# Performance work log

Measured on AMD Instinct MI355X. Metric: run time of the kernel, lower is better.

Reference implementation:

```python
import jax, jax.numpy as jnp
import numpy as np

N_X = 50000      # real nodes
N_MOTIF = 10000  # motif nodes
N = N_X + N_MOTIF
E = 1_920_000    # edges (avg degree 32)
NFEAT = 512
NHID = 256
PAD_N = 65536


def setup_inputs() -> dict:
    key = jax.random.key(0)
    ks = jax.random.split(key, 12)
    x = jax.random.normal(ks[0], (N_X, NFEAT), dtype=jnp.float32)
    motif_emb = jax.random.normal(ks[1], (N_MOTIF, NFEAT), dtype=jnp.float32)
    adj_rows = jax.random.randint(ks[2], (E,), 0, N)
    adj_cols = jax.random.randint(ks[3], (E,), 0, N)
    adj_vals = jax.random.uniform(ks[4], (E,), dtype=jnp.float32)
    # unique scatter positions (torch output[pos_idx]=x with distinct indices)
    pos_idx = jax.random.permutation(ks[5], PAD_N)[:N_X]
    # GraphConvolution params (pygcn style: support = x@W; out = spmm(adj, support) + b)
    s1 = 1.0 / np.sqrt(NHID)
    w1 = jax.random.uniform(ks[6], (NFEAT, NHID), minval=-s1, maxval=s1, dtype=jnp.float32)
    b1 = jax.random.uniform(ks[7], (NHID,), minval=-s1, maxval=s1, dtype=jnp.float32)
    w2 = jax.random.uniform(ks[8], (NHID, NHID), minval=-s1, maxval=s1, dtype=jnp.float32)
    b2 = jax.random.uniform(ks[9], (NHID,), minval=-s1, maxval=s1, dtype=jnp.float32)
    w3 = jax.random.uniform(ks[10], (NHID, NHID), minval=-s1, maxval=s1, dtype=jnp.float32)
    b3 = jax.random.uniform(ks[11], (NHID,), minval=-s1, maxval=s1, dtype=jnp.float32)
    return {"x": x, "motif_emb": motif_emb, "adj_rows": adj_rows, "adj_cols": adj_cols,
            "adj_vals": adj_vals, "pos_idx": pos_idx, "pad_n": PAD_N,
            "w1": w1, "b1": b1, "w2": w2, "b2": b2, "w3": w3, "b3": b3}


def _gcn_layer(h, rows, cols, vals, w, b):
    support = h @ w                                   # [N, nhid]
    msgs = vals[:, None] * support[cols]              # [E, nhid]
    agg = jax.ops.segment_sum(msgs, rows, num_segments=N)  # spmm(adj, support)
    return jax.nn.relu(agg + b)


def reference(x, motif_emb, adj_rows, adj_cols, adj_vals, pos_idx, pad_n,
              w1, b1, w2, b2, w3, b3):
    h = jnp.concatenate((x, motif_emb), axis=0)       # [N, nfeat]
    h = _gcn_layer(h, adj_rows, adj_cols, adj_vals, w1, b1)
    # dropout is identity in eval mode
    h = _gcn_layer(h, adj_rows, adj_cols, adj_vals, w2, b2)
    h = _gcn_layer(h, adj_rows, adj_cols, adj_vals, w3, b3)
    h = h[:N_X]                                       # drop motif nodes
    output = jnp.zeros((pad_n, h.shape[1]), dtype=h.dtype)
    output = output.at[pos_idx].set(h)                # irregular scatter-assign
    return output
```

## Files before the change

### kernel.cpp

```cpp
#include <hip/hip_runtime.h>

#define N_TOTAL 60000
#define N_X     50000
#define N_EDGE  1920000
#define NFEAT   512
#define NHID    256
#define SLOTS   96

typedef __attribute__((ext_vector_type(8))) short bf16x8;
typedef __attribute__((ext_vector_type(4))) float f32x4;
typedef __attribute__((ext_vector_type(4))) unsigned u32x4;

__device__ __forceinline__ unsigned short f2bf(float f) {
    unsigned u = __float_as_uint(f);
    unsigned r = (u + 0x7FFFu + ((u >> 16) & 1u)) >> 16;
    return (unsigned short)r;
}
__device__ __forceinline__ float bf_lo(unsigned u) { return __uint_as_float(u << 16); }
__device__ __forceinline__ float bf_hi(unsigned u) { return __uint_as_float(u & 0xFFFF0000u); }

__global__ __launch_bounds__(256)
void cvt_w_all_kernel(const float* __restrict__ w1, const float* __restrict__ w2,
                      const float* __restrict__ w3, short* __restrict__ w1T,
                      short* __restrict__ w2T, short* __restrict__ w3T)
{
    int n = blockIdx.x;
    for (int k = threadIdx.x; k < NFEAT; k += 256)
        w1T[(size_t)n * NFEAT + k] = (short)f2bf(w1[(size_t)k * NHID + n]);
    for (int k = threadIdx.x; k < NHID; k += 256)
        w2T[(size_t)n * NHID + k] = (short)f2bf(w2[(size_t)k * NHID + n]);
    for (int k = threadIdx.x; k < NHID; k += 256)
        w3T[(size_t)n * NHID + k] = (short)f2bf(w3[(size_t)k * NHID + n]);
}

#define LDA 40

template<bool AF32>
__global__ __launch_bounds__(256)
void gemm_bt_kernel(const float* __restrict__ Af, const float* __restrict__ A2f, int split,
                    const short* __restrict__ Ab, const short* __restrict__ BT,
                    short* __restrict__ C, int M, int K)
{
    __shared__ short As[128 * LDA];
    __shared__ short Bs[128 * LDA];
    const int t    = threadIdx.x;
    const int lane = t & 63;
    const int wave = t >> 6;
    const int wm   = wave & 1;
    const int wn   = wave >> 1;
    const int l16  = lane & 15;
    const int quad = lane >> 4;
    const int bm   = blockIdx.x * 128;
    const int bn   = blockIdx.y * 128;

    f32x4 acc[4][4] = {};

    const int srow = t >> 2;
    const int sch  = t & 3;
    const int frow = t >> 1;
    const int fh   = t & 1;

    for (int kk = 0; kk < K; kk += 32) {
        if (AF32) {
            int row = bm + frow;
            float4 v0 = {}, v1 = {}, v2 = {}, v3 = {};
            if (row < M) {
                const float* src = (row < split) ? (Af + (size_t)row * K)
                                                 : (A2f + (size_t)(row - split) * K);
                const float4* p = (const float4*)(src + kk + fh * 16);
                v0 = p[0]; v1 = p[1]; v2 = p[2]; v3 = p[3];
            }
            short* dst = &As[frow * LDA + fh * 16];
            short tmp[16] = {
                (short)f2bf(v0.x), (short)f2bf(v0.y), (short)f2bf(v0.z), (short)f2bf(v0.w),
                (short)f2bf(v1.x), (short)f2bf(v1.y), (short)f2bf(v1.z), (short)f2bf(v1.w),
                (short)f2bf(v2.x), (short)f2bf(v2.y), (short)f2bf(v2.z), (short)f2bf(v2.w),
                (short)f2bf(v3.x), (short)f2bf(v3.y), (short)f2bf(v3.z), (short)f2bf(v3.w)};
            *(bf16x8*)(dst)     = *(const bf16x8*)&tmp[0];
            *(bf16x8*)(dst + 8) = *(const bf16x8*)&tmp[8];
        } else {
            bf16x8 va0 = {}, va1 = {};
            int r0 = bm + srow, r1 = bm + srow + 64;
            if (r0 < M) va0 = *(const bf16x8*)(Ab + (size_t)r0 * K + kk + sch * 8);
            if (r1 < M) va1 = *(const bf16x8*)(Ab + (size_t)r1 * K + kk + sch * 8);
            *(bf16x8*)&As[srow * LDA + sch * 8]        = va0;
            *(bf16x8*)&As[(srow + 64) * LDA + sch * 8] = va1;
        }
        {
            bf16x8 vb0 = *(const bf16x8*)(BT + (size_t)(bn + srow) * K + kk + sch * 8);
            bf16x8 vb1 = *(const bf16x8*)(BT + (size_t)(bn + srow + 64) * K + kk + sch * 8);
            *(bf16x8*)&Bs[srow * LDA + sch * 8]        = vb0;
            *(bf16x8*)&Bs[(srow + 64) * LDA + sch * 8] = vb1;
        }
        __syncthreads();

        bf16x8 af[4], bfr[4];
        #pragma unroll
        for (int i = 0; i < 4; i++) {
            af[i]  = *(const bf16x8*)&As[(wm * 64 + i * 16 + l16) * LDA + quad * 8];
            bfr[i] = *(const bf16x8*)&Bs[(wn * 64 + i * 16 + l16) * LDA + quad * 8];
        }
        #pragma unroll
        for (int i = 0; i < 4; i++)
            #pragma unroll
            for (int j = 0; j < 4; j++)
                acc[i][j] = __builtin_amdgcn_mfma_f32_16x16x32_bf16(af[i], bfr[j], acc[i][j], 0, 0, 0);
        __syncthreads();
    }

    #pragma unroll
    for (int i = 0; i < 4; i++) {
        #pragma unroll
        for (int r = 0; r < 4; r++) {
            int row = bm + wm * 64 + i * 16 + quad * 4 + r;
            if (row < M) {
                #pragma unroll
                for (int j = 0; j < 4; j++) {
                    int col = bn + wn * 64 + j * 16 + l16;
                    __builtin_nontemporal_store((short)f2bf(acc[i][j][r]),
                                                C + (size_t)row * NHID + col);
                }
            }
        }
    }
}

__global__ __launch_bounds__(256)
void init_cursor_kernel(int* __restrict__ cursor)
{
    int i = blockIdx.x * 256 + threadIdx.x;
    if (i < N_TOTAL) cursor[i] = i * SLOTS;
}

__global__ __launch_bounds__(256)
void scatter_edges_kernel(const int* __restrict__ rows, const int* __restrict__ cols,
                          const float* __restrict__ vals, int* __restrict__ cursor,
                          unsigned* __restrict__ edges)
{
    const int b = blockIdx.x;
    const int g = b & 7;
    const int i = (b >> 3) * 256 + threadIdx.x;
    const int lo = g * (N_TOTAL / 8);
    const int hi = lo + (N_TOTAL / 8);
    int r = __builtin_nontemporal_load(&rows[i]);
    if (r >= lo && r < hi) {
        unsigned rec = (unsigned)cols[i] | ((unsigned)f2bf(vals[i]) << 16);
        int p = atomicAdd(&cursor[r], 1);
        edges[p] = rec;
    }
}

template<int MODE>
__global__ __launch_bounds__(64)
void spmm_relu_kernel(const int* __restrict__ row_end, const unsigned* __restrict__ edges,
                      const u32x4* __restrict__ support, const float* __restrict__ bias,
                      u32x4* __restrict__ out_bf, float* __restrict__ out_f32,
                      const int* __restrict__ pos)
{
    __shared__ unsigned s_edge[64];
    const int r  = blockIdx.x;
    const int t  = threadIdx.x;
    const int eh = t >> 5;
    const int fl = t & 31;
    const int start = r * SLOTS;
    const int end   = row_end[r];
    const u32x4* __restrict__ sb = support + fl;

    float a[8] = {}, b2[8] = {};
    for (int base = start; base < end; base += 64) {
        int j = base + t;
        if (j < end) s_edge[t] = __builtin_nontemporal_load(&edges[j]);
        __syncthreads();
        int cnt = min(64, end - base);
        int i = eh;
        for (; i + 2 < cnt; i += 4) {
            unsigned e0 = s_edge[i], e1 = s_edge[i + 2];
            u32x4 u0 = sb[(size_t)(e0 & 0xFFFFu) * 32];
            u32x4 u1 = sb[(size_t)(e1 & 0xFFFFu) * 32];
            float v0 = bf_hi(e0), v1 = bf_hi(e1);
            #pragma unroll
            for (int k = 0; k < 4; k++) {
                a[2*k]      += v0 * bf_lo(u0[k]);
                a[2*k + 1]  += v0 * bf_hi(u0[k]);
                b2[2*k]     += v1 * bf_lo(u1[k]);
                b2[2*k + 1] += v1 * bf_hi(u1[k]);
            }
        }
        for (; i < cnt; i += 2) {
            unsigned e0 = s_edge[i];
            u32x4 u0 = sb[(size_t)(e0 & 0xFFFFu) * 32];
            float v0 = bf_hi(e0);
            #pragma unroll
            for (int k = 0; k < 4; k++) {
                a[2*k]     += v0 * bf_lo(u0[k]);
                a[2*k + 1] += v0 * bf_hi(u0[k]);
            }
        }
        __syncthreads();
    }

    const f32x4* bb = (const f32x4*)bias + fl * 2;
    f32x4 bv0 = bb[0], bv1 = bb[1];
    float o[8];
    #pragma unroll
    for (int k = 0; k < 8; k++) {
        float s = a[k] + b2[k];
        s += __shfl_xor(s, 32, 64);
        float bk = (k < 4) ? bv0[k] : bv1[k - 4];
        o[k] = fmaxf(s + bk, 0.f);
    }
    if (t < 32) {
        if (MODE == 1) {
            f32x4 q0 = {o[0], o[1], o[2], o[3]};
            f32x4 q1 = {o[4], o[5], o[6], o[7]};
            f32x4* dst = (f32x4*)out_f32 + (size_t)pos[r] * 64 + fl * 2;
            __builtin_nontemporal_store(q0, dst);
            __builtin_nontemporal_store(q1, dst + 1);
        } else {
            u32x4 q;
            #pragma unroll
            for (int k = 0; k < 4; k++)
                q[k] = (unsigned)f2bf(o[2*k]) | ((unsigned)f2bf(o[2*k + 1]) << 16);
            __builtin_nontemporal_store(q, out_bf + (size_t)r * 32 + fl);
        }
    }
}

extern "C" void kernel_launch(void* const* d_in, const int* in_sizes, int n_in,
                              void* d_out, int out_size, void* d_ws, size_t ws_size,
                              hipStream_t stream)
{
    const float* x     = (const float*)d_in[0];
    const float* motif = (const float*)d_in[1];
    const int*   rows  = (const int*)d_in[2];
    const int*   cols  = (const int*)d_in[3];
    const float* vals  = (const float*)d_in[4];
    const int*   pos   = (const int*)d_in[5];
    const float* w1 = (const float*)d_in[7];
    const float* b1 = (const float*)d_in[8];
    const float* w2 = (const float*)d_in[9];
    const float* b2 = (const float*)d_in[10];
    const float* w3 = (const float*)d_in[11];
    const float* b3 = (const float*)d_in[12];
    (void)ws_size; (void)n_in; (void)in_sizes;

    char* ws = (char*)d_ws;
    size_t off = 0;
    short* h_bf     = (short*)(ws + off); off += (size_t)N_TOTAL * NHID * 2;
    short* support  = (short*)(ws + off); off += (size_t)N_TOTAL * NHID * 2;
    short* w1T      = (short*)(ws + off); off += (size_t)NHID * NFEAT * 2;
    short* w2T      = (short*)(ws + off); off += (size_t)NHID * NHID * 2;
    short* w3T      = (short*)(ws + off); off += (size_t)NHID * NHID * 2;
    int* cursor     = (int*)(ws + off);   off += 60032 * 4;
    unsigned* edges = (unsigned*)(ws + off); off += (size_t)N_TOTAL * SLOTS * 4;

    hipMemsetAsync(d_out, 0, (size_t)out_size * sizeof(float), stream);
    cvt_w_all_kernel<<<NHID, 256, 0, stream>>>(w1, w2, w3, w1T, w2T, w3T);
    init_cursor_kernel<<<(N_TOTAL + 255) / 256, 256, 0, stream>>>(cursor);
    scatter_edges_kernel<<<(N_EDGE / 256) * 8, 256, 0, stream>>>(rows, cols, vals, cursor, edges);

    dim3 ggrid((N_TOTAL + 127) / 128, NHID / 128);

    gemm_bt_kernel<true><<<ggrid, 256, 0, stream>>>(x, motif, N_X, nullptr, w1T, support, N_TOTAL, NFEAT);
    spmm_relu_kernel<0><<<N_TOTAL, 64, 0, stream>>>(cursor, edges, (const u32x4*)support, b1,
                                                    (u32x4*)h_bf, nullptr, nullptr);
    gemm_bt_kernel<false><<<ggrid, 256, 0, stream>>>(nullptr, nullptr, 0, h_bf, w2T, support, N_TOTAL, NHID);
    spmm_relu_kernel<0><<<N_TOTAL, 64, 0, stream>>>(cursor, edges, (const u32x4*)support, b2,
                                                    (u32x4*)h_bf, nullptr, nullptr);
    gemm_bt_kernel<false><<<ggrid, 256, 0, stream>>>(nullptr, nullptr, 0, h_bf, w3T, support, N_TOTAL, NHID);
    spmm_relu_kernel<1><<<N_X, 64, 0, stream>>>(cursor, edges, (const u32x4*)support, b3,
                                                nullptr, (float*)d_out, pos);
}
```

Measured before the change: 745.0 us.

## Pack four rows per SpMM block, use wave-local sync, unroll gather by four

The SpMM kernel now runs four rows per 256-thread block, one wavefront per row. Each wave has its own shared edge buffer, and block barriers are replaced with s_waitcnt fences. The gather loop is unrolled to four edges per half-wave so more loads are in flight. The aim is to cut launch and barrier overhead from 60k tiny blocks and to improve memory-level parallelism. The cost is higher register pressure. Correctness now rests on wave-synchronous assumptions: the write to shared memory followed by reads in the same wave, and the hazard where the buffer is reused before all lanes have read it.

Result: no change. 743.9 us (-0.1%).

```diff
diff --git a/kernel.cpp b/kernel.cpp
--- a/kernel.cpp
+++ b/kernel.cpp
@@ -151,33 +151,42 @@
 }
 
 template<int MODE>
-__global__ __launch_bounds__(64)
+__global__ __launch_bounds__(256)
 void spmm_relu_kernel(const int* __restrict__ row_end, const unsigned* __restrict__ edges,
                       const u32x4* __restrict__ support, const float* __restrict__ bias,
                       u32x4* __restrict__ out_bf, float* __restrict__ out_f32,
-                      const int* __restrict__ pos)
-{
-    __shared__ unsigned s_edge[64];
-    const int r  = blockIdx.x;
-    const int t  = threadIdx.x;
-    const int eh = t >> 5;
-    const int fl = t & 31;
+                      const int* __restrict__ pos, int nrows)
+{
+    __shared__ unsigned s_edge[4][64];
+    const int wave = threadIdx.x >> 6;
+    const int lane = threadIdx.x & 63;
+    const int r    = blockIdx.x * 4 + wave;
+    if (r >= nrows) return;
+    const int eh = lane >> 5;
+    const int fl = lane & 31;
     const int start = r * SLOTS;
     const int end   = row_end[r];
     const u32x4* __restrict__ sb = support + fl;
 
     float a[8] = {}, b2[8] = {};
     for (int base = start; base < end; base += 64) {
-        int j = base + t;
-        if (j < end) s_edge[t] = __builtin_nontemporal_load(&edges[j]);
-        __syncthreads();
+        int j = base + lane;
+        asm volatile("s_waitcnt lgkmcnt(0)" ::: "memory");
+        if (j < end) s_edge[wave][lane] = __builtin_nontemporal_load(&edges[j]);
+        asm volatile("s_waitcnt lgkmcnt(0)" ::: "memory");
+        __builtin_amdgcn_sched_barrier(0);
         int cnt = min(64, end - base);
         int i = eh;
-        for (; i + 2 < cnt; i += 4) {
-            unsigned e0 = s_edge[i], e1 = s_edge[i + 2];
+        for (; i + 6 < cnt; i += 8) {
+            unsigned e0 = s_edge[wave][i];
+            unsigned e1 = s_edge[wave][i + 2];
+            unsigned e2 = s_edge[wave][i + 4];
+            unsigned e3 = s_edge[wave][i + 6];
             u32x4 u0 = sb[(size_t)(e0 & 0xFFFFu) * 32];
             u32x4 u1 = sb[(size_t)(e1 & 0xFFFFu) * 32];
-            float v0 = bf_hi(e0), v1 = bf_hi(e1);
+            u32x4 u2 = sb[(size_t)(e2 & 0xFFFFu) * 32];
+            u32x4 u3 = sb[(size_t)(e3 & 0xFFFFu) * 32];
+            float v0 = bf_hi(e0), v1 = bf_hi(e1), v2 = bf_hi(e2), v3 = bf_hi(e3);
             #pragma unroll
             for (int k = 0; k < 4; k++) {
                 a[2*k]      += v0 * bf_lo(u0[k]);
@@ -185,9 +194,29 @@
                 b2[2*k]     += v1 * bf_lo(u1[k]);
                 b2[2*k + 1] += v1 * bf_hi(u1[k]);
             }
+            #pragma unroll
+            for (int k = 0; k < 4; k++) {
+                a[2*k]      += v2 * bf_lo(u2[k]);
+                a[2*k + 1]  += v2 * bf_hi(u2[k]);
+                b2[2*k]     += v3 * bf_lo(u3[k]);
+                b2[2*k + 1] += v3 * bf_hi(u3[k]);
+            }
+        }
+        for (; i + 2 < cnt; i += 4) {
+            unsigned e0 = s_edge[wave][i], e1 = s_edge[wave][i + 2];
+            u32x4 u0 = sb[(size_t)(e0 & 0xFFFFu) * 32];
+            u32x4 u1 = sb[(size_t)(e1 & 0xFFFFu) * 32];
+            float v0 = bf_hi(e0), v1 = bf_hi(e1);
+            #pragma unroll
+            for (int k = 0; k < 4; k++) {
+                a[2*k]      += v0 * bf_lo(u0[k]);
+                a[2*k + 1]  += v0 * bf_hi(u0[k]);
+                b2[2*k]     += v1 * bf_lo(u1[k]);
+                b2[2*k + 1] += v1 * bf_hi(u1[k]);
+            }
         }
         for (; i < cnt; i += 2) {
-            unsigned e0 = s_edge[i];
+            unsigned e0 = s_edge[wave][i];
             u32x4 u0 = sb[(size_t)(e0 & 0xFFFFu) * 32];
             float v0 = bf_hi(e0);
             #pragma unroll
@@ -196,7 +225,6 @@
                 a[2*k + 1] += v0 * bf_hi(u0[k]);
             }
         }
-        __syncthreads();
     }
 
     const f32x4* bb = (const f32x4*)bias + fl * 2;
@@ -209,7 +237,7 @@
         float bk = (k < 4) ? bv0[k] : bv1[k - 4];
         o[k] = fmaxf(s + bk, 0.f);
     }
-    if (t < 32) {
+    if (lane < 32) {
         if (MODE == 1) {
             f32x4 q0 = {o[0], o[1], o[2], o[3]};
             f32x4 q1 = {o[4], o[5], o[6], o[7]};
@@ -262,12 +290,12 @@
     dim3 ggrid((N_TOTAL + 127) / 128, NHID / 128);
 
     gemm_bt_kernel<true><<<ggrid, 256, 0, stream>>>(x, motif, N_X, nullptr, w1T, support, N_TOTAL, NFEAT);
-    spmm_relu_kernel<0><<<N_TOTAL, 64, 0, stream>>>(cursor, edges, (const u32x4*)support, b1,
-                                                    (u32x4*)h_bf, nullptr, nullptr);
+    spmm_relu_kernel<0><<<(N_TOTAL + 3) / 4, 256, 0, stream>>>(cursor, edges, (const u32x4*)support, b1,
+                                                               (u32x4*)h_bf, nullptr, nullptr, N_TOTAL);
     gemm_bt_kernel<false><<<ggrid, 256, 0, stream>>>(nullptr, nullptr, 0, h_bf, w2T, support, N_TOTAL, NHID);
-    spmm_relu_kernel<0><<<N_TOTAL, 64, 0, stream>>>(cursor, edges, (const u32x4*)support, b2,
-                                                    (u32x4*)h_bf, nullptr, nullptr);
+    spmm_relu_kernel<0><<<(N_TOTAL + 3) / 4, 256, 0, stream>>>(cursor, edges, (const u32x4*)support, b2,
+                                                               (u32x4*)h_bf, nullptr, nullptr, N_TOTAL);
     gemm_bt_kernel<false><<<ggrid, 256, 0, stream>>>(nullptr, nullptr, 0, h_bf, w3T, support, N_TOTAL, NHID);
-    spmm_relu_kernel<1><<<N_X, 64, 0, stream>>>(cursor, edges, (const u32x4*)support, b3,
-                                                nullptr, (float*)d_out, pos);
-}
+    spmm_relu_kernel<1><<<(N_X + 3) / 4, 256, 0, stream>>>(cursor, edges, (const u32x4*)support, b3,
+                                                           nullptr, (float*)d_out, pos, N_X);
+}
```
